# Performance work log

Hardware: AMD Instinct MI355X
Metric: run time of the kernel (lower is better)

Reference implementation:

```python
import jax, jax.numpy as jnp
import numpy as np

D_MODEL = 768
N_HEADS = 12
D_K = D_MODEL // N_HEADS
B, S = 2, 2048
EPS = 1e-5  # torch LayerNorm default


def setup_inputs() -> dict:
    key = jax.random.key(0)
    ks = jax.random.split(key, 12)
    sc = 1.0 / np.sqrt(D_MODEL)
    inp = {
        "q": jax.random.normal(ks[0], (B, S, D_MODEL), jnp.float32),
        "k": jax.random.normal(ks[1], (B, S, D_MODEL), jnp.float32),
        "v": jax.random.normal(ks[2], (B, S, D_MODEL), jnp.float32),
        # causal mask: 1 = keep, 0 = masked
        "mask": jnp.tril(jnp.ones((S, S), jnp.int32))[None, None, :, :],
        "Wq": jax.random.normal(ks[3], (D_MODEL, D_MODEL), jnp.float32) * sc,
        "bq": jnp.zeros((D_MODEL,), jnp.float32),
        "Wk": jax.random.normal(ks[4], (D_MODEL, D_MODEL), jnp.float32) * sc,
        "bk": jnp.zeros((D_MODEL,), jnp.float32),
        "Wv": jax.random.normal(ks[5], (D_MODEL, D_MODEL), jnp.float32) * sc,
        "bv": jnp.zeros((D_MODEL,), jnp.float32),
        "Wo": jax.random.normal(ks[6], (D_MODEL, D_MODEL), jnp.float32) * sc,
        "bo": jnp.zeros((D_MODEL,), jnp.float32),
        "gamma": jnp.ones((D_MODEL,), jnp.float32),
        "beta": jnp.zeros((D_MODEL,), jnp.float32),
    }
    return inp


def _layernorm(x, gamma, beta):
    mu = jnp.mean(x, axis=-1, keepdims=True)
    var = jnp.mean(jnp.square(x - mu), axis=-1, keepdims=True)
    return (x - mu) * jax.lax.rsqrt(var + EPS) * gamma + beta


def reference(q, k, v, mask, Wq, bq, Wk, bk, Wv, bv, Wo, bo, gamma, beta):
    residual = q
    # projections + split heads: [B,S,D] -> [B,H,S,Dk]
    def split_heads(x):
        return x.reshape(B, S, N_HEADS, D_K).transpose(0, 2, 1, 3)
    Q = split_heads(q @ Wq.T + bq)
    K = split_heads(k @ Wk.T + bk)
    V = split_heads(v @ Wv.T + bv)
    scores = jnp.einsum("bhqd,bhkd->bhqk", Q, K) / jnp.sqrt(jnp.float32(D_K))
    scores = jnp.where(mask == 0, -jnp.inf, scores)
    attn = jax.nn.softmax(scores, axis=-1)
    # dropout is identity in eval mode
    out = jnp.einsum("bhqk,bhkd->bhqd", attn, V)
    out = out.transpose(0, 2, 1, 3).reshape(B, S, D_MODEL)
    out = out @ Wo.T + bo
    out = _layernorm(residual + out, gamma, beta)
    return (out, attn)
```

## Files before the change

### kernel.cpp

```cpp
#include <hip/hip_runtime.h>
#include <math.h>

typedef __attribute__((ext_vector_type(8))) short bf8_t;
typedef __attribute__((ext_vector_type(4))) float f4_t;

#define MFMA(a,b,c) __builtin_amdgcn_mfma_f32_16x16x32_bf16(a,b,c,0,0,0)

static constexpr int S_ = 2048;
static constexpr size_t QKV_ELEMS = 3145728;
static constexpr size_t W_ELEMS   = 589824;
static constexpr size_t OUT0_ELEMS = 3145728;

__device__ __forceinline__ unsigned short f2bf(float f) {
    union { float f; unsigned u; } v; v.f = f;
    unsigned u = v.u;
    u += 0x7fffu + ((u >> 16) & 1u);
    return (unsigned short)(u >> 16);
}

struct CvtP { const float* s[7]; unsigned short* d[7]; int n[7]; };

__global__ __launch_bounds__(256)
void cvt_all(CvtP p)
{
    const int z = blockIdx.z;
    const int i = (blockIdx.x * 256 + threadIdx.x) * 8;
    if (i >= p.n[z]) return;
    const float* s = p.s[z] + i;
    float4 a = *(const float4*)s, b = *(const float4*)(s + 4);
    uint4 u;
    u.x = (unsigned)f2bf(a.x) | ((unsigned)f2bf(a.y) << 16);
    u.y = (unsigned)f2bf(a.z) | ((unsigned)f2bf(a.w) << 16);
    u.z = (unsigned)f2bf(b.x) | ((unsigned)f2bf(b.y) << 16);
    u.w = (unsigned)f2bf(b.z) | ((unsigned)f2bf(b.w) << 16);
    *(uint4*)(p.d[z] + i) = u;
}

struct GemmP {
    const short* A[3]; const short* W[3]; const float* bias[3];
    void* C[3]; float scale[3]; int mode[3];
};

__global__ __launch_bounds__(256)
void gemm_bf16(GemmP p)
{
    const int z = blockIdx.z;
    const short* __restrict__ A = p.A[z];
    const short* __restrict__ W = p.W[z];
    const float* __restrict__ bias = p.bias[z];
    const float scale = p.scale[z];
    const int mode = p.mode[z];

    __shared__ short As[128 * 40];
    __shared__ short Bs[128 * 40];

    const int t = threadIdx.x;
    const int m0 = blockIdx.y * 128, n0 = blockIdx.x * 128;
    const int w = t >> 6, lane = t & 63, li = lane & 15, qd = lane >> 4;
    const int wm = (w & 1) * 64, wn = (w >> 1) * 64;

    f4_t acc[4][4];
    #pragma unroll
    for (int i = 0; i < 4; ++i)
        #pragma unroll
        for (int j = 0; j < 4; ++j)
            #pragma unroll
            for (int r = 0; r < 4; ++r) acc[i][j][r] = 0.f;

    for (int k0 = 0; k0 < 768; k0 += 32) {
        #pragma unroll
        for (int e = 0; e < 2; ++e) {
            int v = t + e * 256;
            int r = v >> 2, c = (v & 3) * 8;
            *(float4*)&As[r * 40 + c] = *(const float4*)&A[(size_t)(m0 + r) * 768 + k0 + c];
            *(float4*)&Bs[r * 40 + c] = *(const float4*)&W[(size_t)(n0 + r) * 768 + k0 + c];
        }
        __syncthreads();
        bf8_t af[4], bf[4];
        #pragma unroll
        for (int i = 0; i < 4; ++i) af[i] = *(const bf8_t*)&As[(wm + i * 16 + li) * 40 + qd * 8];
        #pragma unroll
        for (int j = 0; j < 4; ++j) bf[j] = *(const bf8_t*)&Bs[(wn + j * 16 + li) * 40 + qd * 8];
        #pragma unroll
        for (int i = 0; i < 4; ++i)
            #pragma unroll
            for (int j = 0; j < 4; ++j)
                acc[i][j] = MFMA(af[i], bf[j], acc[i][j]);
        __syncthreads();
    }

    #pragma unroll
    for (int i = 0; i < 4; ++i) {
        const int row = m0 + wm + i * 16 + qd * 4;
        #pragma unroll
        for (int j = 0; j < 4; ++j) {
            const int col = n0 + wn + j * 16 + li;
            const float bv = bias[col];
            float vals[4];
            #pragma unroll
            for (int r = 0; r < 4; ++r) vals[r] = (acc[i][j][r] + bv) * scale;
            if (mode == 0) {
                #pragma unroll
                for (int r = 0; r < 4; ++r) {
                    const int rr = row + r;
                    int bh = (rr >> 11) * 12 + (col >> 6);
                    ((unsigned short*)p.C[z])[((size_t)bh * 2048 + (rr & 2047)) * 64 + (col & 63)] = f2bf(vals[r]);
                }
            } else if (mode == 1) {
                int bh = (row >> 11) * 12 + (col >> 6);
                ushort4 u;
                u.x = f2bf(vals[0]); u.y = f2bf(vals[1]);
                u.z = f2bf(vals[2]); u.w = f2bf(vals[3]);
                *(ushort4*)&((unsigned short*)p.C[z])[(size_t)(bh * 64 + (col & 63)) * 2048 + (row & 2047)] = u;
            } else {
                #pragma unroll
                for (int r = 0; r < 4; ++r)
                    ((float*)p.C[z])[(size_t)(row + r) * 768 + col] = vals[r];
            }
        }
    }
}

__global__ __launch_bounds__(64)
void attn_fused(const short* __restrict__ Qb, const short* __restrict__ Kb,
                const short* __restrict__ Vt, float* __restrict__ attn,
                unsigned short* __restrict__ AO)
{
    const int sidx = blockIdx.x;
    const int qt = 31 - (sidx >> 2);
    const int ws = sidx & 3;
    const int bh = blockIdx.y;
    const int lane = threadIdx.x;
    const int li = lane & 15, qd = lane >> 4;

    __shared__ short Ps[16 * 72];

    const int q0 = qt * 64 + ws * 16;
    const short* Qp = Qb + ((size_t)bh * 2048 + q0 + li) * 64;
    const bf8_t qf0 = *(const bf8_t*)&Qp[qd * 8];
    const bf8_t qf1 = *(const bf8_t*)&Qp[32 + qd * 8];

    const short* Kbh = Kb + (size_t)bh * 2048 * 64;
    const short* Vbh = Vt + (size_t)bh * 64 * 2048;
    float* attnp = attn + (size_t)bh * 2048 * 2048;

    const float NEG = -1e30f;
    float m_[4] = {NEG, NEG, NEG, NEG}, l_[4] = {0.f, 0.f, 0.f, 0.f};

    bf8_t kc0[4], kc1[4], kn0[4], kn1[4];
    #pragma unroll
    for (int sub = 0; sub < 4; ++sub) {
        const short* Kr = Kbh + (size_t)(sub * 16 + li) * 64;
        kc0[sub] = *(const bf8_t*)&Kr[qd * 8];
        kc1[sub] = *(const bf8_t*)&Kr[32 + qd * 8];
    }

    for (int kt = 0; kt <= qt; ++kt) {
        if (kt < qt) {
            #pragma unroll
            for (int sub = 0; sub < 4; ++sub) {
                const short* Kr = Kbh + (size_t)((kt + 1) * 64 + sub * 16 + li) * 64;
                kn0[sub] = *(const bf8_t*)&Kr[qd * 8];
                kn1[sub] = *(const bf8_t*)&Kr[32 + qd * 8];
            }
        }
        f4_t c[4];
        #pragma unroll
        for (int sub = 0; sub < 4; ++sub) {
            f4_t z; z[0] = z[1] = z[2] = z[3] = 0.f;
            z = MFMA(qf0, kc0[sub], z);
            z = MFMA(qf1, kc1[sub], z);
            c[sub] = z;
        }
        if (kt == qt) {
            #pragma unroll
            for (int sub = 0; sub < 4; ++sub)
                #pragma unroll
                for (int r = 0; r < 4; ++r)
                    if (sub * 16 + li > ws * 16 + qd * 4 + r) c[sub][r] = NEG;
        }
        #pragma unroll
        for (int r = 0; r < 4; ++r) {
            float tm = fmaxf(fmaxf(c[0][r], c[1][r]), fmaxf(c[2][r], c[3][r]));
            float nm = fmaxf(m_[r], tm);
            float s = __expf(c[0][r] - nm) + __expf(c[1][r] - nm)
                    + __expf(c[2][r] - nm) + __expf(c[3][r] - nm);
            l_[r] = l_[r] * __expf(m_[r] - nm) + s;
            m_[r] = nm;
        }
        #pragma unroll
        for (int sub = 0; sub < 4; ++sub) { kc0[sub] = kn0[sub]; kc1[sub] = kn1[sub]; }
    }

    float invl[4];
    #pragma unroll
    for (int r = 0; r < 4; ++r) {
        float mg = m_[r];
        mg = fmaxf(mg, __shfl_xor(mg, 1, 64));
        mg = fmaxf(mg, __shfl_xor(mg, 2, 64));
        mg = fmaxf(mg, __shfl_xor(mg, 4, 64));
        mg = fmaxf(mg, __shfl_xor(mg, 8, 64));
        float lg = l_[r] * __expf(m_[r] - mg);
        lg += __shfl_xor(lg, 1, 64);
        lg += __shfl_xor(lg, 2, 64);
        lg += __shfl_xor(lg, 4, 64);
        lg += __shfl_xor(lg, 8, 64);
        m_[r] = mg;
        invl[r] = 1.f / lg;
    }

    f4_t o[4];
    #pragma unroll
    for (int d = 0; d < 4; ++d)
        #pragma unroll
        for (int r = 0; r < 4; ++r) o[d][r] = 0.f;

    #pragma unroll
    for (int sub = 0; sub < 4; ++sub) {
        const short* Kr = Kbh + (size_t)(sub * 16 + li) * 64;
        kc0[sub] = *(const bf8_t*)&Kr[qd * 8];
        kc1[sub] = *(const bf8_t*)&Kr[32 + qd * 8];
    }
    for (int kt = 0; kt <= qt; ++kt) {
        if (kt < qt) {
            #pragma unroll
            for (int sub = 0; sub < 4; ++sub) {
                const short* Kr = Kbh + (size_t)((kt + 1) * 64 + sub * 16 + li) * 64;
                kn0[sub] = *(const bf8_t*)&Kr[qd * 8];
                kn1[sub] = *(const bf8_t*)&Kr[32 + qd * 8];
            }
        }
        bf8_t vb[2][4];
        #pragma unroll
        for (int h = 0; h < 2; ++h)
            #pragma unroll
            for (int d = 0; d < 4; ++d)
                vb[h][d] = *(const bf8_t*)&Vbh[(size_t)(d * 16 + li) * 2048 + kt * 64 + h * 32 + qd * 8];

        f4_t c[4];
        #pragma unroll
        for (int sub = 0; sub < 4; ++sub) {
            f4_t z; z[0] = z[1] = z[2] = z[3] = 0.f;
            z = MFMA(qf0, kc0[sub], z);
            z = MFMA(qf1, kc1[sub], z);
            c[sub] = z;
        }
        if (kt == qt) {
            #pragma unroll
            for (int sub = 0; sub < 4; ++sub)
                #pragma unroll
                for (int r = 0; r < 4; ++r)
                    if (sub * 16 + li > ws * 16 + qd * 4 + r) c[sub][r] = NEG;
        }
        #pragma unroll
        for (int sub = 0; sub < 4; ++sub)
            #pragma unroll
            for (int r = 0; r < 4; ++r) {
                const float pe = __expf(c[sub][r] - m_[r]) * invl[r];
                attnp[(size_t)(q0 + qd * 4 + r) * 2048 + kt * 64 + sub * 16 + li] = pe;
                Ps[(qd * 4 + r) * 72 + sub * 16 + li] = (short)f2bf(pe);
            }
        #pragma unroll
        for (int h = 0; h < 2; ++h) {
            bf8_t pa = *(const bf8_t*)&Ps[li * 72 + h * 32 + qd * 8];
            #pragma unroll
            for (int d = 0; d < 4; ++d)
                o[d] = MFMA(pa, vb[h][d], o[d]);
        }
        #pragma unroll
        for (int sub = 0; sub < 4; ++sub) { kc0[sub] = kn0[sub]; kc1[sub] = kn1[sub]; }
    }

    const int w4 = (31 - qt) * 16;
    const float4 z4 = make_float4(0.f, 0.f, 0.f, 0.f);
    for (int r = 0; r < 16; ++r) {
        float* rp = &attnp[(size_t)(q0 + r) * 2048 + (qt + 1) * 64];
        for (int c = lane; c < w4; c += 64)
            *(float4*)&rp[c * 4] = z4;
    }

    const int b = bh / 12, h_ = bh % 12;
    #pragma unroll
    for (int d = 0; d < 4; ++d)
        #pragma unroll
        for (int r = 0; r < 4; ++r)
            AO[(size_t)(b * 2048 + q0 + qd * 4 + r) * 768 + h_ * 64 + d * 16 + li] = f2bf(o[d][r]);
}

__global__ __launch_bounds__(256)
void ln_kernel(const float* __restrict__ resid, const float* __restrict__ proj,
               const float* __restrict__ gamma, const float* __restrict__ beta,
               float* __restrict__ out)
{
    __shared__ float red[4];
    const int row = blockIdx.x, t = threadIdx.x;
    const size_t base = (size_t)row * 768;
    float x[3];
    float s = 0.f;
    #pragma unroll
    for (int e = 0; e < 3; ++e) {
        int j = t + e * 256;
        x[e] = resid[base + j] + proj[base + j];
        s += x[e];
    }
    #pragma unroll
    for (int off = 1; off < 64; off <<= 1) s += __shfl_xor(s, off, 64);
    if ((t & 63) == 0) red[t >> 6] = s;
    __syncthreads();
    s = red[0] + red[1] + red[2] + red[3];
    const float mu = s * (1.f / 768.f);
    float vs = 0.f;
    #pragma unroll
    for (int e = 0; e < 3; ++e) { float d = x[e] - mu; vs += d * d; }
    __syncthreads();
    #pragma unroll
    for (int off = 1; off < 64; off <<= 1) vs += __shfl_xor(vs, off, 64);
    if ((t & 63) == 0) red[t >> 6] = vs;
    __syncthreads();
    vs = red[0] + red[1] + red[2] + red[3];
    const float inv = rsqrtf(vs * (1.f / 768.f) + 1e-5f);
    #pragma unroll
    for (int e = 0; e < 3; ++e) {
        int j = t + e * 256;
        out[base + j] = (x[e] - mu) * inv * gamma[j] + beta[j];
    }
}

extern "C" void kernel_launch(void* const* d_in, const int* in_sizes, int n_in,
                              void* d_out, int out_size, void* d_ws, size_t ws_size,
                              hipStream_t stream)
{
    const float* q     = (const float*)d_in[0];
    const float* k     = (const float*)d_in[1];
    const float* v     = (const float*)d_in[2];
    const float* Wq    = (const float*)d_in[4];
    const float* bq    = (const float*)d_in[5];
    const float* Wk    = (const float*)d_in[6];
    const float* bk    = (const float*)d_in[7];
    const float* Wv    = (const float*)d_in[8];
    const float* bv    = (const float*)d_in[9];
    const float* Wo    = (const float*)d_in[10];
    const float* bo    = (const float*)d_in[11];
    const float* gamma = (const float*)d_in[12];
    const float* beta  = (const float*)d_in[13];

    float* out  = (float*)d_out;
    float* attn = out + OUT0_ELEMS;

    short* qc  = (short*)d_ws;
    short* kc  = qc + QKV_ELEMS;
    short* vc  = kc + QKV_ELEMS;
    short* wqc = vc + QKV_ELEMS;
    short* wkc = wqc + W_ELEMS;
    short* wvc = wkc + W_ELEMS;
    short* woc = wvc + W_ELEMS;
    short* Qb  = woc + W_ELEMS;
    short* Kb  = Qb + QKV_ELEMS;
    short* Vt  = Kb + QKV_ELEMS;
    short* AO  = Vt + QKV_ELEMS;
    float* P   = (float*)(AO + QKV_ELEMS);

    CvtP cp;
    cp.s[0] = q;  cp.d[0] = (unsigned short*)qc;  cp.n[0] = (int)QKV_ELEMS;
    cp.s[1] = k;  cp.d[1] = (unsigned short*)kc;  cp.n[1] = (int)QKV_ELEMS;
    cp.s[2] = v;  cp.d[2] = (unsigned short*)vc;  cp.n[2] = (int)QKV_ELEMS;
    cp.s[3] = Wq; cp.d[3] = (unsigned short*)wqc; cp.n[3] = (int)W_ELEMS;
    cp.s[4] = Wk; cp.d[4] = (unsigned short*)wkc; cp.n[4] = (int)W_ELEMS;
    cp.s[5] = Wv; cp.d[5] = (unsigned short*)wvc; cp.n[5] = (int)W_ELEMS;
    cp.s[6] = Wo; cp.d[6] = (unsigned short*)woc; cp.n[6] = (int)W_ELEMS;
    cvt_all<<<dim3(1536, 1, 7), 256, 0, stream>>>(cp);

    GemmP gp;
    gp.A[0] = qc; gp.W[0] = wqc; gp.bias[0] = bq; gp.C[0] = Qb; gp.scale[0] = 0.125f; gp.mode[0] = 0;
    gp.A[1] = kc; gp.W[1] = wkc; gp.bias[1] = bk; gp.C[1] = Kb; gp.scale[1] = 1.f;    gp.mode[1] = 0;
    gp.A[2] = vc; gp.W[2] = wvc; gp.bias[2] = bv; gp.C[2] = Vt; gp.scale[2] = 1.f;    gp.mode[2] = 1;
    gemm_bf16<<<dim3(6, 32, 3), 256, 0, stream>>>(gp);

    attn_fused<<<dim3(128, 24), 64, 0, stream>>>(Qb, Kb, Vt, attn, (unsigned short*)AO);

    GemmP gp2;
    gp2.A[0] = AO; gp2.W[0] = woc; gp2.bias[0] = bo; gp2.C[0] = P; gp2.scale[0] = 1.f; gp2.mode[0] = 2;
    gp2.A[1] = gp2.A[2] = AO; gp2.W[1] = gp2.W[2] = woc; gp2.bias[1] = gp2.bias[2] = bo;
    gp2.C[1] = gp2.C[2] = P; gp2.scale[1] = gp2.scale[2] = 1.f; gp2.mode[1] = gp2.mode[2] = 2;
    gemm_bf16<<<dim3(6, 32, 1), 256, 0, stream>>>(gp2);

    ln_kernel<<<dim3(4096), 256, 0, stream>>>(q, P, gamma, beta, out);
}
```

Before: 708.8 us.

## Share K/V tiles across four waves via double-buffered swizzled LDS

The attention kernel now runs four 16-row query waves per 256-thread block instead of one wave per block. Each block cooperatively loads 64x64 K and V tiles into double-buffered, XOR-swizzled shared memory, with the next tile prefetched into registers while the current one is computed. This cuts redundant global K/V reads by four and avoids bank conflicts, at the cost of per-tile __syncthreads and fewer, larger blocks (768 instead of 3072), which may hurt load balance on the causal triangle.

```diff
diff --git a/kernel.cpp b/kernel.cpp
--- a/kernel.cpp
+++ b/kernel.cpp
@@ -121,19 +121,21 @@
     }
 }
 
-__global__ __launch_bounds__(64)
+__global__ __launch_bounds__(256)
 void attn_fused(const short* __restrict__ Qb, const short* __restrict__ Kb,
                 const short* __restrict__ Vt, float* __restrict__ attn,
                 unsigned short* __restrict__ AO)
 {
-    const int sidx = blockIdx.x;
-    const int qt = 31 - (sidx >> 2);
-    const int ws = sidx & 3;
+    const int qt = 31 - blockIdx.x;
     const int bh = blockIdx.y;
-    const int lane = threadIdx.x;
+    const int t = threadIdx.x;
+    const int ws = t >> 6;
+    const int lane = t & 63;
     const int li = lane & 15, qd = lane >> 4;
 
-    __shared__ short Ps[16 * 72];
+    __shared__ short Ks[2][4096];
+    __shared__ short Vs[2][4096];
+    __shared__ short Ps[4][1024];
 
     const int q0 = qt * 64 + ws * 16;
     const short* Qp = Qb + ((size_t)bh * 2048 + q0 + li) * 64;
@@ -143,53 +145,66 @@
     const short* Kbh = Kb + (size_t)bh * 2048 * 64;
     const short* Vbh = Vt + (size_t)bh * 64 * 2048;
     float* attnp = attn + (size_t)bh * 2048 * 2048;
+    short* Psw = Ps[ws];
+
+    const int r0 = t >> 3, c0 = t & 7;
+    const int csw = ((c0 ^ (r0 & 7)) << 3);
+    const int lsw = li & 7;
 
     const float NEG = -1e30f;
     float m_[4] = {NEG, NEG, NEG, NEG}, l_[4] = {0.f, 0.f, 0.f, 0.f};
 
-    bf8_t kc0[4], kc1[4], kn0[4], kn1[4];
-    #pragma unroll
-    for (int sub = 0; sub < 4; ++sub) {
-        const short* Kr = Kbh + (size_t)(sub * 16 + li) * 64;
-        kc0[sub] = *(const bf8_t*)&Kr[qd * 8];
-        kc1[sub] = *(const bf8_t*)&Kr[32 + qd * 8];
-    }
-
-    for (int kt = 0; kt <= qt; ++kt) {
-        if (kt < qt) {
+    {
+        float4 ka = *(const float4*)&Kbh[(size_t)r0 * 64 + (c0 << 3)];
+        float4 kb_ = *(const float4*)&Kbh[(size_t)(r0 + 32) * 64 + (c0 << 3)];
+        *(float4*)&Ks[0][r0 * 64 + csw] = ka;
+        *(float4*)&Ks[0][(r0 + 32) * 64 + csw] = kb_;
+        int cur = 0;
+        for (int kt = 0; kt <= qt; ++kt) {
+            float4 na, nb;
+            if (kt < qt) {
+                na = *(const float4*)&Kbh[(size_t)((kt + 1) * 64 + r0) * 64 + (c0 << 3)];
+                nb = *(const float4*)&Kbh[(size_t)((kt + 1) * 64 + r0 + 32) * 64 + (c0 << 3)];
+            }
+            __syncthreads();
+            const short* Kc = Ks[cur];
+            bf8_t kf0[4], kf1[4];
             #pragma unroll
             for (int sub = 0; sub < 4; ++sub) {
-                const short* Kr = Kbh + (size_t)((kt + 1) * 64 + sub * 16 + li) * 64;
-                kn0[sub] = *(const bf8_t*)&Kr[qd * 8];
-                kn1[sub] = *(const bf8_t*)&Kr[32 + qd * 8];
+                const int kr = sub * 16 + li;
+                kf0[sub] = *(const bf8_t*)&Kc[kr * 64 + ((qd ^ lsw) << 3)];
+                kf1[sub] = *(const bf8_t*)&Kc[kr * 64 + (((4 + qd) ^ lsw) << 3)];
+            }
+            f4_t c[4];
+            #pragma unroll
+            for (int sub = 0; sub < 4; ++sub) {
+                f4_t z; z[0] = z[1] = z[2] = z[3] = 0.f;
+                z = MFMA(qf0, kf0[sub], z);
+                z = MFMA(qf1, kf1[sub], z);
+                c[sub] = z;
+            }
+            if (kt == qt) {
+                #pragma unroll
+                for (int sub = 0; sub < 4; ++sub)
+                    #pragma unroll
+                    for (int r = 0; r < 4; ++r)
+                        if (sub * 16 + li > ws * 16 + qd * 4 + r) c[sub][r] = NEG;
+            }
+            #pragma unroll
+            for (int r = 0; r < 4; ++r) {
+                float tm = fmaxf(fmaxf(c[0][r], c[1][r]), fmaxf(c[2][r], c[3][r]));
+                float nm = fmaxf(m_[r], tm);
+                float s = __expf(c[0][r] - nm) + __expf(c[1][r] - nm)
+                        + __expf(c[2][r] - nm) + __expf(c[3][r] - nm);
+                l_[r] = l_[r] * __expf(m_[r] - nm) + s;
+                m_[r] = nm;
+            }
+            if (kt < qt) {
+                *(float4*)&Ks[cur ^ 1][r0 * 64 + csw] = na;
+                *(float4*)&Ks[cur ^ 1][(r0 + 32) * 64 + csw] = nb;
+                cur ^= 1;
             }
         }
-        f4_t c[4];
-        #pragma unroll
-        for (int sub = 0; sub < 4; ++sub) {
-            f4_t z; z[0] = z[1] = z[2] = z[3] = 0.f;
-            z = MFMA(qf0, kc0[sub], z);
-            z = MFMA(qf1, kc1[sub], z);
-            c[sub] = z;
-        }
-        if (kt == qt) {
-            #pragma unroll
-            for (int sub = 0; sub < 4; ++sub)
-                #pragma unroll
-                for (int r = 0; r < 4; ++r)
-                    if (sub * 16 + li > ws * 16 + qd * 4 + r) c[sub][r] = NEG;
-        }
-        #pragma unroll
-        for (int r = 0; r < 4; ++r) {
-            float tm = fmaxf(fmaxf(c[0][r], c[1][r]), fmaxf(c[2][r], c[3][r]));
-            float nm = fmaxf(m_[r], tm);
-            float s = __expf(c[0][r] - nm) + __expf(c[1][r] - nm)
-                    + __expf(c[2][r] - nm) + __expf(c[3][r] - nm);
-            l_[r] = l_[r] * __expf(m_[r] - nm) + s;
-            m_[r] = nm;
-        }
-        #pragma unroll
-        for (int sub = 0; sub < 4; ++sub) { kc0[sub] = kn0[sub]; kc1[sub] = kn1[sub]; }
     }
 
     float invl[4];
@@ -215,68 +230,85 @@
         #pragma unroll
         for (int r = 0; r < 4; ++r) o[d][r] = 0.f;
 
-    #pragma unroll
-    for (int sub = 0; sub < 4; ++sub) {
-        const short* Kr = Kbh + (size_t)(sub * 16 + li) * 64;
-        kc0[sub] = *(const bf8_t*)&Kr[qd * 8];
-        kc1[sub] = *(const bf8_t*)&Kr[32 + qd * 8];
-    }
-    for (int kt = 0; kt <= qt; ++kt) {
-        if (kt < qt) {
+    {
+        float4 ka = *(const float4*)&Kbh[(size_t)r0 * 64 + (c0 << 3)];
+        float4 kb_ = *(const float4*)&Kbh[(size_t)(r0 + 32) * 64 + (c0 << 3)];
+        float4 va = *(const float4*)&Vbh[(size_t)r0 * 2048 + (c0 << 3)];
+        float4 vc_ = *(const float4*)&Vbh[(size_t)(r0 + 32) * 2048 + (c0 << 3)];
+        __syncthreads();
+        *(float4*)&Ks[0][r0 * 64 + csw] = ka;
+        *(float4*)&Ks[0][(r0 + 32) * 64 + csw] = kb_;
+        *(float4*)&Vs[0][r0 * 64 + csw] = va;
+        *(float4*)&Vs[0][(r0 + 32) * 64 + csw] = vc_;
+        int cur = 0;
+        for (int kt = 0; kt <= qt; ++kt) {
+            float4 nka, nkb, nva, nvb;
+            if (kt < qt) {
+                nka = *(const float4*)&Kbh[(size_t)((kt + 1) * 64 + r0) * 64 + (c0 << 3)];
+                nkb = *(const float4*)&Kbh[(size_t)((kt + 1) * 64 + r0 + 32) * 64 + (c0 << 3)];
+                nva = *(const float4*)&Vbh[(size_t)r0 * 2048 + (kt + 1) * 64 + (c0 << 3)];
+                nvb = *(const float4*)&Vbh[(size_t)(r0 + 32) * 2048 + (kt + 1) * 64 + (c0 << 3)];
+            }
+            __syncthreads();
+            const short* Kc = Ks[cur];
+            const short* Vc = Vs[cur];
+            bf8_t kf0[4], kf1[4];
             #pragma unroll
             for (int sub = 0; sub < 4; ++sub) {
-                const short* Kr = Kbh + (size_t)((kt + 1) * 64 + sub * 16 + li) * 64;
-                kn0[sub] = *(const bf8_t*)&Kr[qd * 8];
-                kn1[sub] = *(const bf8_t*)&Kr[32 + qd * 8];
+                const int kr = sub * 16 + li;
+                kf0[sub] = *(const bf8_t*)&Kc[kr * 64 + ((qd ^ lsw) << 3)];
+                kf1[sub] = *(const bf8_t*)&Kc[kr * 64 + (((4 + qd) ^ lsw) << 3)];
+            }
+            f4_t c[4];
+            #pragma unroll
+            for (int sub = 0; sub < 4; ++sub) {
+                f4_t z; z[0] = z[1] = z[2] = z[3] = 0.f;
+                z = MFMA(qf0, kf0[sub], z);
+                z = MFMA(qf1, kf1[sub], z);
+                c[sub] = z;
+            }
+            if (kt == qt) {
+                #pragma unroll
+                for (int sub = 0; sub < 4; ++sub)
+                    #pragma unroll
+                    for (int r = 0; r < 4; ++r)
+                        if (sub * 16 + li > ws * 16 + qd * 4 + r) c[sub][r] = NEG;
+            }
+            #pragma unroll
+            for (int sub = 0; sub < 4; ++sub)
+                #pragma unroll
+                for (int r = 0; r < 4; ++r) {
+                    const float pe = __expf(c[sub][r] - m_[r]) * invl[r];
+                    attnp[(size_t)(q0 + qd * 4 + r) * 2048 + kt * 64 + sub * 16 + li] = pe;
+                    const int prow = qd * 4 + r;
+                    const int pcol = sub * 16 + li;
+                    Psw[prow * 64 + (((pcol >> 3) ^ (prow & 7)) << 3) + (pcol & 7)] = (short)f2bf(pe);
+                }
+            #pragma unroll
+            for (int h = 0; h < 2; ++h) {
+                bf8_t pa = *(const bf8_t*)&Psw[li * 64 + (((h * 4 + qd) ^ lsw) << 3)];
+                #pragma unroll
+                for (int d = 0; d < 4; ++d) {
+                    bf8_t vf = *(const bf8_t*)&Vc[(d * 16 + li) * 64 + (((h * 4 + qd) ^ lsw) << 3)];
+                    o[d] = MFMA(pa, vf, o[d]);
+                }
+            }
+            if (kt < qt) {
+                *(float4*)&Ks[cur ^ 1][r0 * 64 + csw] = nka;
+                *(float4*)&Ks[cur ^ 1][(r0 + 32) * 64 + csw] = nkb;
+                *(float4*)&Vs[cur ^ 1][r0 * 64 + csw] = nva;
+                *(float4*)&Vs[cur ^ 1][(r0 + 32) * 64 + csw] = nvb;
+                cur ^= 1;
             }
         }
-        bf8_t vb[2][4];
-        #pragma unroll
-        for (int h = 0; h < 2; ++h)
-            #pragma unroll
-            for (int d = 0; d < 4; ++d)
-                vb[h][d] = *(const bf8_t*)&Vbh[(size_t)(d * 16 + li) * 2048 + kt * 64 + h * 32 + qd * 8];
-
-        f4_t c[4];
-        #pragma unroll
-        for (int sub = 0; sub < 4; ++sub) {
-            f4_t z; z[0] = z[1] = z[2] = z[3] = 0.f;
-            z = MFMA(qf0, kc0[sub], z);
-            z = MFMA(qf1, kc1[sub], z);
-            c[sub] = z;
-        }
-        if (kt == qt) {
-            #pragma unroll
-            for (int sub = 0; sub < 4; ++sub)
-                #pragma unroll
-                for (int r = 0; r < 4; ++r)
-                    if (sub * 16 + li > ws * 16 + qd * 4 + r) c[sub][r] = NEG;
-        }
-        #pragma unroll
-        for (int sub = 0; sub < 4; ++sub)
-            #pragma unroll
-            for (int r = 0; r < 4; ++r) {
-                const float pe = __expf(c[sub][r] - m_[r]) * invl[r];
-                attnp[(size_t)(q0 + qd * 4 + r) * 2048 + kt * 64 + sub * 16 + li] = pe;
-                Ps[(qd * 4 + r) * 72 + sub * 16 + li] = (short)f2bf(pe);
-            }
-        #pragma unroll
-        for (int h = 0; h < 2; ++h) {
-            bf8_t pa = *(const bf8_t*)&Ps[li * 72 + h * 32 + qd * 8];
-            #pragma unroll
-            for (int d = 0; d < 4; ++d)
-                o[d] = MFMA(pa, vb[h][d], o[d]);
-        }
-        #pragma unroll
-        for (int sub = 0; sub < 4; ++sub) { kc0[sub] = kn0[sub]; kc1[sub] = kn1[sub]; }
     }
 
     const int w4 = (31 - qt) * 16;
     const float4 z4 = make_float4(0.f, 0.f, 0.f, 0.f);
     for (int r = 0; r < 16; ++r) {
         float* rp = &attnp[(size_t)(q0 + r) * 2048 + (qt + 1) * 64];
-        for (int c = lane; c < w4; c += 64)
-            *(float4*)&rp[c * 4] = z4;
+        for (int cc = lane; cc < w4; cc += 64)
+            *(float4*)&rp[cc * 4] = z4;
     }
 
     const int b = bh / 12, h_ = bh % 12;
@@ -376,7 +408,7 @@
     gp.A[2] = vc; gp.W[2] = wvc; gp.bias[2] = bv; gp.C[2] = Vt; gp.scale[2] = 1.f;    gp.mode[2] = 1;
     gemm_bf16<<<dim3(6, 32, 3), 256, 0, stream>>>(gp);
 
-    attn_fused<<<dim3(128, 24), 64, 0, stream>>>(Qb, Kb, Vt, attn, (unsigned short*)AO);
+    attn_fused<<<dim3(32, 24), 256, 0, stream>>>(Qb, Kb, Vt, attn, (unsigned short*)AO);
 
     GemmP gp2;
     gp2.A[0] = AO; gp2.W[0] = woc; gp2.bias[0] = bo; gp2.C[0] = P; gp2.scale[0] = 1.f; gp2.mode[0] = 2;
```

After: 595.5 us. 1.19x faster.

## Store Q/K/V in MFMA-fragment order, use 4-wave attention blocks and direct-to-LDS GEMM loads

Applied to the files above, without the earlier changes.

The projection GEMM epilogue now writes Q, K and V in a tiled layout that matches the MFMA fragment order, so the attention kernel's K/V fragment loads become contiguous 16-byte reads. The attention kernel packs four 16-row query strips into one 256-thread block and snake-orders the blocks over (query tile, head) to balance the causal work. It also XOR-swizzles the P staging buffer in LDS to avoid bank conflicts. The GEMM moves global-to-LDS staging to global_load_lds with unpadded tiles, which may bring back LDS bank conflicts on the fragment reads.

```diff
diff --git a/kernel.cpp b/kernel.cpp
--- a/kernel.cpp
+++ b/kernel.cpp
@@ -16,6 +16,12 @@
     unsigned u = v.u;
     u += 0x7fffu + ((u >> 16) & 1u);
     return (unsigned short)(u >> 16);
+}
+
+__device__ __forceinline__ void gload_lds16(const short* g, short* l) {
+    __builtin_amdgcn_global_load_lds((const __attribute__((address_space(1))) void*)g,
+                                     (__attribute__((address_space(3))) void*)l,
+                                     16, 0, 0);
 }
 
 struct CvtP { const float* s[7]; unsigned short* d[7]; int n[7]; };
@@ -51,8 +57,8 @@
     const float scale = p.scale[z];
     const int mode = p.mode[z];
 
-    __shared__ short As[128 * 40];
-    __shared__ short Bs[128 * 40];
+    __shared__ short As[128 * 32];
+    __shared__ short Bs[128 * 32];
 
     const int t = threadIdx.x;
     const int m0 = blockIdx.y * 128, n0 = blockIdx.x * 128;
@@ -70,17 +76,17 @@
     for (int k0 = 0; k0 < 768; k0 += 32) {
         #pragma unroll
         for (int e = 0; e < 2; ++e) {
-            int v = t + e * 256;
-            int r = v >> 2, c = (v & 3) * 8;
-            *(float4*)&As[r * 40 + c] = *(const float4*)&A[(size_t)(m0 + r) * 768 + k0 + c];
-            *(float4*)&Bs[r * 40 + c] = *(const float4*)&W[(size_t)(n0 + r) * 768 + k0 + c];
+            const int ch = t + e * 256;
+            const int r = ch >> 2, c = (ch & 3) << 3;
+            gload_lds16(&A[(size_t)(m0 + r) * 768 + k0 + c], &As[ch << 3]);
+            gload_lds16(&W[(size_t)(n0 + r) * 768 + k0 + c], &Bs[ch << 3]);
         }
         __syncthreads();
         bf8_t af[4], bf[4];
         #pragma unroll
-        for (int i = 0; i < 4; ++i) af[i] = *(const bf8_t*)&As[(wm + i * 16 + li) * 40 + qd * 8];
-        #pragma unroll
-        for (int j = 0; j < 4; ++j) bf[j] = *(const bf8_t*)&Bs[(wn + j * 16 + li) * 40 + qd * 8];
+        for (int i = 0; i < 4; ++i) af[i] = *(const bf8_t*)&As[(wm + i * 16 + li) * 32 + qd * 8];
+        #pragma unroll
+        for (int j = 0; j < 4; ++j) bf[j] = *(const bf8_t*)&Bs[(wn + j * 16 + li) * 32 + qd * 8];
         #pragma unroll
         for (int i = 0; i < 4; ++i)
             #pragma unroll
@@ -100,18 +106,32 @@
             #pragma unroll
             for (int r = 0; r < 4; ++r) vals[r] = (acc[i][j][r] + bv) * scale;
             if (mode == 0) {
+                const int head = col >> 6;
+                const int cq = col & 63;
+                const int half = cq >> 5, qd_ = (cq >> 3) & 3, e = cq & 7;
                 #pragma unroll
                 for (int r = 0; r < 4; ++r) {
                     const int rr = row + r;
-                    int bh = (rr >> 11) * 12 + (col >> 6);
-                    ((unsigned short*)p.C[z])[((size_t)bh * 2048 + (rr & 2047)) * 64 + (col & 63)] = f2bf(vals[r]);
+                    const int bh = (rr >> 11) * 12 + head;
+                    const int s = rr & 2047;
+                    const int kt = s >> 6, sub = (s >> 4) & 3, li_ = s & 15;
+                    const size_t idx = ((((size_t)bh * 32 + kt) * 2 + half) * 4 + sub) * 512
+                                     + li_ * 32 + qd_ * 8 + e;
+                    ((unsigned short*)p.C[z])[idx] = f2bf(vals[r]);
                 }
             } else if (mode == 1) {
-                int bh = (row >> 11) * 12 + (col >> 6);
+                const int head = col >> 6;
+                const int rr = row;
+                const int bh = (rr >> 11) * 12 + head;
+                const int s = rr & 2047;
+                const int kt = s >> 6, h = (s >> 5) & 1, qd_ = (s >> 3) & 3, e0 = s & 7;
+                const int d_ = (col & 63) >> 4, li_ = col & 15;
+                const size_t idx = (((((size_t)bh * 32 + kt) * 2 + h) * 4 + d_) * 16 + li_) * 32
+                                 + qd_ * 8 + e0;
                 ushort4 u;
                 u.x = f2bf(vals[0]); u.y = f2bf(vals[1]);
                 u.z = f2bf(vals[2]); u.w = f2bf(vals[3]);
-                *(ushort4*)&((unsigned short*)p.C[z])[(size_t)(bh * 64 + (col & 63)) * 2048 + (row & 2047)] = u;
+                *(ushort4*)&((unsigned short*)p.C[z])[idx] = u;
             } else {
                 #pragma unroll
                 for (int r = 0; r < 4; ++r)
@@ -121,75 +141,83 @@
     }
 }
 
-__global__ __launch_bounds__(64)
-void attn_fused(const short* __restrict__ Qb, const short* __restrict__ Kb,
-                const short* __restrict__ Vt, float* __restrict__ attn,
+__global__ __launch_bounds__(256, 3)
+void attn_fused(const short* __restrict__ Qf, const short* __restrict__ Kf,
+                const short* __restrict__ Vf, float* __restrict__ attn,
                 unsigned short* __restrict__ AO)
 {
-    const int sidx = blockIdx.x;
-    const int qt = 31 - (sidx >> 2);
-    const int ws = sidx & 3;
-    const int bh = blockIdx.y;
-    const int lane = threadIdx.x;
+    __shared__ short Ps[4][1024];
+
+    const int B = blockIdx.x;
+    const int s_ = B & 255, rr_ = B >> 8;
+    const int item = (rr_ == 0) ? s_ : (rr_ == 1) ? (511 - s_) : (512 + s_);
+    const int qt = 31 - (item / 24);
+    const int bh = item % 24;
+
+    const int t = threadIdx.x;
+    const int ws = t >> 6;
+    const int lane = t & 63;
     const int li = lane & 15, qd = lane >> 4;
-
-    __shared__ short Ps[16 * 72];
+    const int lq = li * 32 + qd * 8;
+    const int lsw = li & 7;
+    const float NEG = -1e30f;
 
     const int q0 = qt * 64 + ws * 16;
-    const short* Qp = Qb + ((size_t)bh * 2048 + q0 + li) * 64;
-    const bf8_t qf0 = *(const bf8_t*)&Qp[qd * 8];
-    const bf8_t qf1 = *(const bf8_t*)&Qp[32 + qd * 8];
-
-    const short* Kbh = Kb + (size_t)bh * 2048 * 64;
-    const short* Vbh = Vt + (size_t)bh * 64 * 2048;
+    const short* Qbase = Qf + ((((size_t)bh * 32 + qt) * 2) * 4 + ws) * 512 + lq;
+    const bf8_t qf0 = *(const bf8_t*)&Qbase[0];
+    const bf8_t qf1 = *(const bf8_t*)&Qbase[2048];
+
+    const short* Kfb = Kf + (size_t)bh * 131072;
+    const short* Vfb = Vf + (size_t)bh * 131072;
     float* attnp = attn + (size_t)bh * 2048 * 2048;
-
-    const float NEG = -1e30f;
+    short* Psw = Ps[ws];
+
     float m_[4] = {NEG, NEG, NEG, NEG}, l_[4] = {0.f, 0.f, 0.f, 0.f};
 
     bf8_t kc0[4], kc1[4], kn0[4], kn1[4];
-    #pragma unroll
-    for (int sub = 0; sub < 4; ++sub) {
-        const short* Kr = Kbh + (size_t)(sub * 16 + li) * 64;
-        kc0[sub] = *(const bf8_t*)&Kr[qd * 8];
-        kc1[sub] = *(const bf8_t*)&Kr[32 + qd * 8];
-    }
-
-    for (int kt = 0; kt <= qt; ++kt) {
-        if (kt < qt) {
+
+    {
+        #pragma unroll
+        for (int sub = 0; sub < 4; ++sub) {
+            kc0[sub] = *(const bf8_t*)&Kfb[sub * 512 + lq];
+            kc1[sub] = *(const bf8_t*)&Kfb[2048 + sub * 512 + lq];
+        }
+        for (int kt = 0; kt <= qt; ++kt) {
+            if (kt < qt) {
+                const short* Kn = Kfb + (size_t)(kt + 1) * 4096;
+                #pragma unroll
+                for (int sub = 0; sub < 4; ++sub) {
+                    kn0[sub] = *(const bf8_t*)&Kn[sub * 512 + lq];
+                    kn1[sub] = *(const bf8_t*)&Kn[2048 + sub * 512 + lq];
+                }
+            }
+            f4_t c[4];
             #pragma unroll
             for (int sub = 0; sub < 4; ++sub) {
-                const short* Kr = Kbh + (size_t)((kt + 1) * 64 + sub * 16 + li) * 64;
-                kn0[sub] = *(const bf8_t*)&Kr[qd * 8];
-                kn1[sub] = *(const bf8_t*)&Kr[32 + qd * 8];
-            }
-        }
-        f4_t c[4];
-        #pragma unroll
-        for (int sub = 0; sub < 4; ++sub) {
-            f4_t z; z[0] = z[1] = z[2] = z[3] = 0.f;
-            z = MFMA(qf0, kc0[sub], z);
-            z = MFMA(qf1, kc1[sub], z);
-            c[sub] = z;
-        }
-        if (kt == qt) {
-            #pragma unroll
-            for (int sub = 0; sub < 4; ++sub)
-                #pragma unroll
-                for (int r = 0; r < 4; ++r)
-                    if (sub * 16 + li > ws * 16 + qd * 4 + r) c[sub][r] = NEG;
-        }
-        #pragma unroll
-        for (int r = 0; r < 4; ++r) {
-            float tm = fmaxf(fmaxf(c[0][r], c[1][r]), fmaxf(c[2][r], c[3][r]));
-            float nm = fmaxf(m_[r], tm);
-            float s = __expf(c[0][r] - nm) + __expf(c[1][r] - nm)
-                    + __expf(c[2][r] - nm) + __expf(c[3][r] - nm);
-            l_[r] = l_[r] * __expf(m_[r] - nm) + s;
-            m_[r] = nm;
-        }
-        #pragma unroll
-        for (int sub = 0; sub < 4; ++sub) { kc0[sub] = kn0[sub]; kc1[sub] = kn1[sub]; }
+                f4_t z; z[0] = z[1] = z[2] = z[3] = 0.f;
+                z = MFMA(qf0, kc0[sub], z);
+                z = MFMA(qf1, kc1[sub], z);
+                c[sub] = z;
+            }
+            if (kt == qt) {
+                #pragma unroll
+                for (int sub = 0; sub < 4; ++sub)
+                    #pragma unroll
+                    for (int r = 0; r < 4; ++r)
+                        if (sub * 16 + li > ws * 16 + qd * 4 + r) c[sub][r] = NEG;
+            }
+            #pragma unroll
+            for (int r = 0; r < 4; ++r) {
+                float tm = fmaxf(fmaxf(c[0][r], c[1][r]), fmaxf(c[2][r], c[3][r]));
+                float nm = fmaxf(m_[r], tm);
+                float s = __expf(c[0][r] - nm) + __expf(c[1][r] - nm)
+                        + __expf(c[2][r] - nm) + __expf(c[3][r] - nm);
+                l_[r] = l_[r] * __expf(m_[r] - nm) + s;
+                m_[r] = nm;
+            }
+            #pragma unroll
+            for (int sub = 0; sub < 4; ++sub) { kc0[sub] = kn0[sub]; kc1[sub] = kn1[sub]; }
+        }
     }
 
     float invl[4];
@@ -215,68 +243,71 @@
         #pragma unroll
         for (int r = 0; r < 4; ++r) o[d][r] = 0.f;
 
-    #pragma unroll
-    for (int sub = 0; sub < 4; ++sub) {
-        const short* Kr = Kbh + (size_t)(sub * 16 + li) * 64;
-        kc0[sub] = *(const bf8_t*)&Kr[qd * 8];
-        kc1[sub] = *(const bf8_t*)&Kr[32 + qd * 8];
-    }
-    for (int kt = 0; kt <= qt; ++kt) {
-        if (kt < qt) {
+    {
+        #pragma unroll
+        for (int sub = 0; sub < 4; ++sub) {
+            kc0[sub] = *(const bf8_t*)&Kfb[sub * 512 + lq];
+            kc1[sub] = *(const bf8_t*)&Kfb[2048 + sub * 512 + lq];
+        }
+        for (int kt = 0; kt <= qt; ++kt) {
+            const short* Vt_ = Vfb + (size_t)kt * 4096;
+            bf8_t vb[2][4];
+            #pragma unroll
+            for (int h = 0; h < 2; ++h)
+                #pragma unroll
+                for (int d = 0; d < 4; ++d)
+                    vb[h][d] = *(const bf8_t*)&Vt_[h * 2048 + d * 512 + lq];
+            if (kt < qt) {
+                const short* Kn = Kfb + (size_t)(kt + 1) * 4096;
+                #pragma unroll
+                for (int sub = 0; sub < 4; ++sub) {
+                    kn0[sub] = *(const bf8_t*)&Kn[sub * 512 + lq];
+                    kn1[sub] = *(const bf8_t*)&Kn[2048 + sub * 512 + lq];
+                }
+            }
+            f4_t c[4];
             #pragma unroll
             for (int sub = 0; sub < 4; ++sub) {
-                const short* Kr = Kbh + (size_t)((kt + 1) * 64 + sub * 16 + li) * 64;
-                kn0[sub] = *(const bf8_t*)&Kr[qd * 8];
-                kn1[sub] = *(const bf8_t*)&Kr[32 + qd * 8];
-            }
-        }
-        bf8_t vb[2][4];
-        #pragma unroll
-        for (int h = 0; h < 2; ++h)
-            #pragma unroll
-            for (int d = 0; d < 4; ++d)
-                vb[h][d] = *(const bf8_t*)&Vbh[(size_t)(d * 16 + li) * 2048 + kt * 64 + h * 32 + qd * 8];
-
-        f4_t c[4];
-        #pragma unroll
-        for (int sub = 0; sub < 4; ++sub) {
-            f4_t z; z[0] = z[1] = z[2] = z[3] = 0.f;
-            z = MFMA(qf0, kc0[sub], z);
-            z = MFMA(qf1, kc1[sub], z);
-            c[sub] = z;
-        }
-        if (kt == qt) {
+                f4_t z; z[0] = z[1] = z[2] = z[3] = 0.f;
+                z = MFMA(qf0, kc0[sub], z);
+                z = MFMA(qf1, kc1[sub], z);
+                c[sub] = z;
+            }
+            if (kt == qt) {
+                #pragma unroll
+                for (int sub = 0; sub < 4; ++sub)
+                    #pragma unroll
+                    for (int r = 0; r < 4; ++r)
+                        if (sub * 16 + li > ws * 16 + qd * 4 + r) c[sub][r] = NEG;
+            }
             #pragma unroll
             for (int sub = 0; sub < 4; ++sub)
                 #pragma unroll
-                for (int r = 0; r < 4; ++r)
-                    if (sub * 16 + li > ws * 16 + qd * 4 + r) c[sub][r] = NEG;
-        }
-        #pragma unroll
-        for (int sub = 0; sub < 4; ++sub)
-            #pragma unroll
-            for (int r = 0; r < 4; ++r) {
-                const float pe = __expf(c[sub][r] - m_[r]) * invl[r];
-                attnp[(size_t)(q0 + qd * 4 + r) * 2048 + kt * 64 + sub * 16 + li] = pe;
-                Ps[(qd * 4 + r) * 72 + sub * 16 + li] = (short)f2bf(pe);
-            }
-        #pragma unroll
-        for (int h = 0; h < 2; ++h) {
-            bf8_t pa = *(const bf8_t*)&Ps[li * 72 + h * 32 + qd * 8];
-            #pragma unroll
-            for (int d = 0; d < 4; ++d)
-                o[d] = MFMA(pa, vb[h][d], o[d]);
-        }
-        #pragma unroll
-        for (int sub = 0; sub < 4; ++sub) { kc0[sub] = kn0[sub]; kc1[sub] = kn1[sub]; }
+                for (int r = 0; r < 4; ++r) {
+                    const float pe = __expf(c[sub][r] - m_[r]) * invl[r];
+                    attnp[(size_t)(q0 + qd * 4 + r) * 2048 + kt * 64 + sub * 16 + li] = pe;
+                    const int prow = qd * 4 + r;
+                    const int pcol = sub * 16 + li;
+                    Psw[prow * 64 + (((pcol >> 3) ^ (prow & 7)) << 3) + (pcol & 7)] = (short)f2bf(pe);
+                }
+            #pragma unroll
+            for (int h = 0; h < 2; ++h) {
+                bf8_t pa = *(const bf8_t*)&Psw[li * 64 + (((h * 4 + qd) ^ lsw) << 3)];
+                #pragma unroll
+                for (int d = 0; d < 4; ++d)
+                    o[d] = MFMA(pa, vb[h][d], o[d]);
+            }
+            #pragma unroll
+            for (int sub = 0; sub < 4; ++sub) { kc0[sub] = kn0[sub]; kc1[sub] = kn1[sub]; }
+        }
     }
 
     const int w4 = (31 - qt) * 16;
     const float4 z4 = make_float4(0.f, 0.f, 0.f, 0.f);
     for (int r = 0; r < 16; ++r) {
         float* rp = &attnp[(size_t)(q0 + r) * 2048 + (qt + 1) * 64];
-        for (int c = lane; c < w4; c += 64)
-            *(float4*)&rp[c * 4] = z4;
+        for (int cc = lane; cc < w4; cc += 64)
+            *(float4*)&rp[cc * 4] = z4;
     }
 
     const int b = bh / 12, h_ = bh % 12;
@@ -376,7 +407,7 @@
     gp.A[2] = vc; gp.W[2] = wvc; gp.bias[2] = bv; gp.C[2] = Vt; gp.scale[2] = 1.f;    gp.mode[2] = 1;
     gemm_bf16<<<dim3(6, 32, 3), 256, 0, stream>>>(gp);
 
-    attn_fused<<<dim3(128, 24), 64, 0, stream>>>(Qb, Kb, Vt, attn, (unsigned short*)AO);
+    attn_fused<<<dim3(768), 256, 0, stream>>>(Qb, Kb, Vt, attn, (unsigned short*)AO);
 
     GemmP gp2;
     gp2.A[0] = AO; gp2.W[0] = woc; gp2.bias[0] = bo; gp2.C[0] = P; gp2.scale[0] = 1.f; gp2.mode[0] = 2;
```

Result: faster. 629.1 us (-11.3%).
